# Optimization experiments

Measured on AMD Instinct MI355X. Metric: run time of the kernel, lower is better.

The kernel has to match this reference:

```python
import jax, jax.numpy as jnp
import numpy as np

NX = 2048
NY = 2048
K0 = 0.15                      # standard HW box wavenumber -> L = 2*pi/K0
KAPPA = 1.0
ALPHA = 1.0
DN = 0.001
DOMEGA = 0.001
K2_MIN = 1e-12


def _grid():
    L = 2.0 * np.pi / K0
    dx = L / NX
    dy = L / NY
    kx = (2.0 * np.pi * np.fft.fftfreq(NX, d=dx)).astype(np.float32)[:, None]  # [NX,1]
    ky = (2.0 * np.pi * np.fft.fftfreq(NY, d=dy)).astype(np.float32)[None, :]  # [1,NY]
    k2 = kx * kx + ky * ky
    # 2/3-rule dealias mask
    kx_max = np.abs(kx).max()
    ky_max = np.abs(ky).max()
    mask = ((np.abs(kx) <= (2.0 / 3.0) * kx_max) & (np.abs(ky) <= (2.0 / 3.0) * ky_max))
    return jnp.asarray(kx), jnp.asarray(ky), jnp.asarray(k2), jnp.asarray(mask)

KX, KY, K2, DEALIAS = _grid()


def _inv_laplacian_hat(w_hat):
    # phi_hat = -w_hat / k2, zeroing the (near-)zero modes
    safe_k2 = jnp.where(K2 > K2_MIN, K2, 1.0)
    return jnp.where(K2 > K2_MIN, -w_hat / safe_k2, 0.0)


def _bracket_spectral(phi_hat, f_hat):
    # J = d_x phi * d_y f - d_y phi * d_x f, dealiased with 2/3 mask
    dphix = jnp.fft.ifft2(1j * KX * phi_hat).real
    dphiy = jnp.fft.ifft2(1j * KY * phi_hat).real
    dfx = jnp.fft.ifft2(1j * KX * f_hat).real
    dfy = jnp.fft.ifft2(1j * KY * f_hat).real
    j = dphix * dfy - dphiy * dfx
    return jnp.fft.ifft2(DEALIAS * jnp.fft.fft2(j)).real


def setup_inputs() -> dict:
    key = jax.random.key(0)
    k1, k2 = jax.random.split(key)
    n = 0.1 * jax.random.normal(k1, (NX, NY), dtype=jnp.float32)
    omega = 0.1 * jax.random.normal(k2, (NX, NY), dtype=jnp.float32)
    return {"n": n, "omega": omega}


def reference(n, omega):
    n_hat = jnp.fft.fft2(n)
    w_hat = jnp.fft.fft2(omega)
    phi_hat = _inv_laplacian_hat(w_hat)
    phi = jnp.fft.ifft2(phi_hat).real

    adv_n = _bracket_spectral(phi_hat, n_hat)
    adv_w = _bracket_spectral(phi_hat, w_hat)

    dphi_dy = jnp.fft.ifft2(1j * KY * phi_hat).real
    dn_dy = jnp.fft.ifft2(1j * KY * n_hat).real

    drive_n = -KAPPA * dphi_dy
    drive_w = -KAPPA * dn_dy
    couple = ALPHA * (phi - n)

    lap_n = jnp.fft.ifft2(-K2 * n_hat).real
    lap_w = jnp.fft.ifft2(-K2 * w_hat).real

    dn = -adv_n + drive_n + couple + DN * lap_n
    dw = -adv_w + drive_w + couple + DOMEGA * lap_w
    return jnp.stack([dn, dw])  # [2, NX, NY]
```

## Files before the change

kernel.cpp:

```cpp
#include <hip/hip_runtime.h>
#include <hip/hip_fp16.h>
#include <math.h>


#define NF 2048
#define HALF 1024
#define K0F 0.15f
#define DEAL_LIM 682

typedef float2 cplx;
typedef __half2 ch;

__device__ __forceinline__ ch toh(cplx v){ return __float22half2_rn(make_float2(v.x, v.y)); }
__device__ __forceinline__ cplx toc(ch h){ float2 f = __half22float2(h); return make_float2(f.x, f.y); }

__device__ __forceinline__ int sw(int i){ return i ^ ((i>>4)&15) ^ ((i>>8)&15); }
__device__ __forceinline__ cplx cmul(cplx a, cplx b){ return make_float2(a.x*b.x - a.y*b.y, a.x*b.y + a.y*b.x); }
__device__ __forceinline__ cplx cadd(cplx a, cplx b){ return make_float2(a.x+b.x, a.y+b.y); }
__device__ __forceinline__ cplx csub(cplx a, cplx b){ return make_float2(a.x-b.x, a.y-b.y); }
template<int SIGN> __device__ __forceinline__ cplx rot90(cplx z){
  return (SIGN>0)? make_float2(-z.y,z.x) : make_float2(z.y,-z.x); }
__device__ __forceinline__ void lput(cplx* L, int i, cplx v){ L[sw(i)] = v; }
__device__ __forceinline__ cplx lget(const cplx* L, int i){ return L[sw(i)]; }

__device__ __forceinline__ int xcd_chunk(int bid, int nwg){
  return (bid & 7) * (nwg >> 3) + (bid >> 3);
}

template<int SIGN, int TPR, int M>
__device__ __forceinline__ void stage8_ip(cplx* X, int t) {
  constexpr int BPT = 256 / TPR;
  const float ang = (float)SIGN * 0.0030679615757712824f;
  cplx a[BPT][8];
#pragma unroll
  for (int u = 0; u < BPT; ++u) {
    const int b = t + u * TPR;
#pragma unroll
    for (int k = 0; k < 8; ++k) a[u][k] = X[sw(b + 256 * k)];
  }
  __syncthreads();
#pragma unroll
  for (int u = 0; u < BPT; ++u) {
    const int b = t + u * TPR;
    const int i = b & (M - 1);
    const int jm = b - i;
    cplx a0=a[u][0], a1=a[u][1], a2=a[u][2], a3=a[u][3],
         a4=a[u][4], a5=a[u][5], a6=a[u][6], a7=a[u][7];
    cplx t0=cadd(a0,a4), t1=csub(a0,a4), t2=cadd(a2,a6), t3=rot90<SIGN>(csub(a2,a6));
    cplx E0=cadd(t0,t2), E2=csub(t0,t2), E1=cadd(t1,t3), E3=csub(t1,t3);
    cplx u0=cadd(a1,a5), u1=csub(a1,a5), u2=cadd(a3,a7), u3=rot90<SIGN>(csub(a3,a7));
    cplx O0=cadd(u0,u2), O2=csub(u0,u2), O1=cadd(u1,u3), O3=csub(u1,u3);
    const float hh = 0.70710678118654752440f;
    O1 = cmul(O1, make_float2(hh, (float)SIGN*hh));
    O2 = rot90<SIGN>(O2);
    O3 = cmul(O3, make_float2(-hh, (float)SIGN*hh));
    cplx y0=cadd(E0,O0), y4=csub(E0,O0);
    cplx y1=cadd(E1,O1), y5=csub(E1,O1);
    cplx y2=cadd(E2,O2), y6=csub(E2,O2);
    cplx y3=cadd(E3,O3), y7=csub(E3,O3);
    float sn, cs;
    __sincosf(ang * (float)jm, &sn, &cs);
    cplx w1 = make_float2(cs, sn);
    cplx w2 = cmul(w1,w1), w3 = cmul(w2,w1), w4 = cmul(w2,w2);
    cplx w5 = cmul(w3,w2), w6 = cmul(w3,w3), w7 = cmul(w4,w3);
    const int o = 8*jm + i;
    X[sw(o)]       = y0;
    X[sw(o+M)]     = cmul(y1,w1);
    X[sw(o+2*M)]   = cmul(y2,w2);
    X[sw(o+3*M)]   = cmul(y3,w3);
    X[sw(o+4*M)]   = cmul(y4,w4);
    X[sw(o+5*M)]   = cmul(y5,w5);
    X[sw(o+6*M)]   = cmul(y6,w6);
    X[sw(o+7*M)]   = cmul(y7,w7);
  }
  __syncthreads();
}

template<int SIGN, int TPR>
__device__ __forceinline__ void stage4_ip(cplx* X, int t){
  constexpr int QPT = 512 / TPR;
  cplx a[QPT][4];
#pragma unroll
  for (int u=0; u<QPT; ++u){
    const int b = t + u*TPR;
#pragma unroll
    for (int k=0;k<4;++k) a[u][k] = X[sw(b + 512*k)];
  }
  __syncthreads();
#pragma unroll
  for (int u=0; u<QPT; ++u){
    const int b = t + u*TPR;
    cplx a0=a[u][0], a1=a[u][1], a2=a[u][2], a3=a[u][3];
    cplx t0=cadd(a0,a2), t1=csub(a0,a2), t2=cadd(a1,a3), t3=rot90<SIGN>(csub(a1,a3));
    X[sw(b)]       = cadd(t0,t2);
    X[sw(b+512)]   = cadd(t1,t3);
    X[sw(b+1024)]  = csub(t0,t2);
    X[sw(b+1536)]  = csub(t1,t3);
  }
  __syncthreads();
}

template<int SIGN, int TPR>
__device__ __forceinline__ void fft_ip(cplx* X, int t){
  __syncthreads();
  stage8_ip<SIGN,TPR,1>(X,t);
  stage8_ip<SIGN,TPR,8>(X,t);
  stage8_ip<SIGN,TPR,64>(X,t);
  stage4_ip<SIGN,TPR>(X,t);
}

__device__ __forceinline__ void unpack_point(cplx a, cplx b,
    float kxv, float kyv, float kxp, float kyp,
    cplx& s1, cplx& s2, cplx& s3, cplx& s4) {
  cplx nh = make_float2(0.5f*(a.x + b.x),  0.5f*(a.y - b.y));
  cplx wh = make_float2(0.5f*(a.y + b.y), -0.5f*(a.x - b.x));
  float k2 = kxv*kxv + kyv*kyv;
  float pinv = (k2 > 1e-12f) ? (-1.0f/k2) : 0.0f;
  cplx ph = make_float2(wh.x*pinv, wh.y*pinv);
  s1 = make_float2(-kxp*ph.y - kyp*ph.x, kxp*ph.x - kyp*ph.y);
  s2 = make_float2(-kxp*nh.y - kyp*nh.x, kxp*nh.x - kyp*nh.y);
  s3 = make_float2(-kxp*wh.y - kyp*wh.x, kxp*wh.x - kyp*wh.y);
  float dnc = 0.001f * k2;
  cplx Ln = make_float2( kyp*ph.y + (ph.x - nh.x) - dnc*nh.x,
                        -kyp*ph.x + (ph.y - nh.y) - dnc*nh.y);
  cplx Lw = make_float2( kyp*nh.y + (ph.x - nh.x) - dnc*wh.x,
                        -kyp*nh.x + (ph.y - nh.y) - dnc*wh.y);
  s4 = make_float2(Ln.x - Lw.y, Ln.y + Lw.x);
}


__global__ void __launch_bounds__(512) k_fwd_pack_T(const float* __restrict__ nIn,
                                                    const float* __restrict__ wIn,
                                                    cplx* __restrict__ out) {
  __shared__ cplx L[4*NF];
  const int tid = threadIdx.x;
  const int lb = xcd_chunk(blockIdx.x, gridDim.x);
  const int xb = lb*4;
#pragma unroll
  for (int u=0; u<4; ++u){
    int f = tid + u*512;
    int r = f >> 9;
    int p = f & 511;
    float4 nv = ((const float4*)(nIn + (size_t)(xb+r)*NF))[p];
    float4 wv = ((const float4*)(wIn + (size_t)(xb+r)*NF))[p];
    cplx* Lr = L + r*NF;
    lput(Lr, 4*p+0, make_float2(nv.x, wv.x));
    lput(Lr, 4*p+1, make_float2(nv.y, wv.y));
    lput(Lr, 4*p+2, make_float2(nv.z, wv.z));
    lput(Lr, 4*p+3, make_float2(nv.w, wv.w));
  }
  const int row = tid >> 7, t = tid & 127;
  fft_ip<-1,128>(L + row*NF, t);
  float4* o4 = (float4*)out;
#pragma unroll
  for (int u=0; u<8; ++u){
    int f = tid + u*512;
    int ky = f >> 1;
    int xp = f & 1;
    cplx a = lget(L + (2*xp)*NF, ky);
    cplx b = lget(L + (2*xp+1)*NF, ky);
    o4[(size_t)ky*(NF/2) + lb*2 + xp] = make_float4(a.x,a.y,b.x,b.y);
  }
}

__global__ void __launch_bounds__(512) k_unpackS(const cplx* __restrict__ in,
                                                 ch* __restrict__ S1, ch* __restrict__ S2,
                                                 ch* __restrict__ S3, ch* __restrict__ S4) {
  __shared__ cplx F0[NF], F1[NF];
  const int tid = threadIdx.x;
  const int b = xcd_chunk(blockIdx.x, gridDim.x);
  const int kyA = b;
  const int kyB = (b == 0) ? HALF : NF - b;
  const int half = tid >> 8;
  const int t = tid & 255;
  cplx* Fm = half ? F1 : F0;
  {
    const cplx* g = in + (size_t)(half ? kyB : kyA)*NF;
#pragma unroll
    for (int u=0; u<4; ++u){
      int p = t + u*256;
      float4 v = ((const float4*)g)[p];
      lput(Fm, 2*p,   make_float2(v.x,v.y));
      lput(Fm, 2*p+1, make_float2(v.z,v.w));
    }
    fft_ip<-1,256>(Fm, t);
  }
  const cplx* Fp = (b == 0) ? (const cplx*)Fm : (half ? F0 : F1);
  const int kyM = half ? kyB : kyA;
  const int sy = (kyM < HALF) ? kyM : kyM - NF;
  const float kyv = K0F * (float)sy;
  const float kyp = (kyM == HALF) ? 0.0f : kyv;
  const float sc = 1.0f/(float)NF;
  const size_t rbase = (size_t)kyM * NF;
#pragma unroll
  for (int u=0; u<8; ++u){
    int kx = t + u*256;
    int kx2 = (NF - kx) & (NF - 1);
    int sx = (kx < HALF) ? kx : kx - NF;
    float kxv = K0F * (float)sx;
    float kxp = (kx == HALF) ? 0.0f : kxv;
    cplx s1,s2,s3,s4;
    unpack_point(lget(Fm,kx), lget(Fp,kx2), kxv, kyv, kxp, kyp, s1,s2,s3,s4);
    S1[rbase+kx] = toh(make_float2(sc*s1.x, sc*s1.y));
    S2[rbase+kx] = toh(make_float2(sc*s2.x, sc*s2.y));
    S3[rbase+kx] = toh(make_float2(sc*s3.x, sc*s3.y));
    S4[rbase+kx] = toh(make_float2(sc*s4.x, sc*s4.y));
  }
}

__global__ void __launch_bounds__(512) k_inv2(const ch* __restrict__ in0,
                                              const ch* __restrict__ in1,
                                              ch* __restrict__ out0,
                                              ch* __restrict__ out1) {
  __shared__ cplx L[4*NF];
  const int tid = threadIdx.x;
  const int lb = xcd_chunk(blockIdx.x, gridDim.x);
  const ch* in = blockIdx.y ? in1 : in0;
  ch* out = blockIdx.y ? out1 : out0;
  const int rb = lb*4;
#pragma unroll
  for (int u=0; u<4; ++u){
    int f = tid + u*512;
    int r = f >> 9, p = f & 511;
    uint4 v = ((const uint4*)(in + (size_t)(rb+r)*NF))[p];
    cplx* Lr = L + r*NF;
    lput(Lr, 4*p+0, toc(*(ch*)&v.x));
    lput(Lr, 4*p+1, toc(*(ch*)&v.y));
    lput(Lr, 4*p+2, toc(*(ch*)&v.z));
    lput(Lr, 4*p+3, toc(*(ch*)&v.w));
  }
  const int row = tid >> 7, t = tid & 127;
  fft_ip<1,128>(L + row*NF, t);
  uint4* o16 = (uint4*)out;
#pragma unroll
  for (int u=0; u<4; ++u){
    int q = tid + u*512;
    ch h0 = toh(lget(L + 0*NF, q));
    ch h1 = toh(lget(L + 1*NF, q));
    ch h2 = toh(lget(L + 2*NF, q));
    ch h3 = toh(lget(L + 3*NF, q));
    uint4 v;
    v.x = *(unsigned*)&h0; v.y = *(unsigned*)&h1;
    v.z = *(unsigned*)&h2; v.w = *(unsigned*)&h3;
    o16[(size_t)q*(NF/4) + lb] = v;
  }
}

__global__ void __launch_bounds__(256) k_bracket(const ch* __restrict__ T1,
                                                 const ch* __restrict__ T2,
                                                 const ch* __restrict__ T3,
                                                 ch* __restrict__ out) {
  __shared__ cplx A[NF];
  const int t = threadIdx.x;
  const size_t base = (size_t)blockIdx.x * NF;
#pragma unroll
  for (int u=0; u<2; ++u){
    int p = t + u*256;
    uint4 v = ((const uint4*)(T1 + base))[p];
    lput(A, 4*p+0, toc(*(ch*)&v.x)); lput(A, 4*p+1, toc(*(ch*)&v.y));
    lput(A, 4*p+2, toc(*(ch*)&v.z)); lput(A, 4*p+3, toc(*(ch*)&v.w));
  }
  fft_ip<1,256>(A, t);
  cplx dphi[8];
#pragma unroll
  for (int u=0; u<8; ++u) dphi[u] = lget(A, t + u*256);
  __syncthreads();
#pragma unroll
  for (int u=0; u<2; ++u){
    int p = t + u*256;
    uint4 v = ((const uint4*)(T2 + base))[p];
    lput(A, 4*p+0, toc(*(ch*)&v.x)); lput(A, 4*p+1, toc(*(ch*)&v.y));
    lput(A, 4*p+2, toc(*(ch*)&v.z)); lput(A, 4*p+3, toc(*(ch*)&v.w));
  }
  fft_ip<1,256>(A, t);
  float jn[8];
#pragma unroll
  for (int u=0; u<8; ++u){
    cplx dd = lget(A, t + u*256);
    jn[u] = dphi[u].x*dd.y - dphi[u].y*dd.x;
  }
  __syncthreads();
#pragma unroll
  for (int u=0; u<2; ++u){
    int p = t + u*256;
    uint4 v = ((const uint4*)(T3 + base))[p];
    lput(A, 4*p+0, toc(*(ch*)&v.x)); lput(A, 4*p+1, toc(*(ch*)&v.y));
    lput(A, 4*p+2, toc(*(ch*)&v.z)); lput(A, 4*p+3, toc(*(ch*)&v.w));
  }
  fft_ip<1,256>(A, t);
  const float sc2 = 1.0f/((float)NF*(float)NF);
#pragma unroll
  for (int u=0; u<8; ++u){
    int c = t + u*256;
    cplx dd = lget(A, c);
    float jw = dphi[u].x*dd.y - dphi[u].y*dd.x;
    lput(A, c, make_float2(sc2*jn[u], sc2*jw));
  }
  fft_ip<-1,256>(A, t);
  uint4* o16 = (uint4*)(out + base);
#pragma unroll
  for (int u=0; u<2; ++u){
    int p = t + u*256;
    if (p <= 170 || p >= 341) {
      ch h0 = toh(lget(A, 4*p+0));
      ch h1 = toh(lget(A, 4*p+1));
      ch h2 = toh(lget(A, 4*p+2));
      ch h3 = toh(lget(A, 4*p+3));
      uint4 v;
      v.x = *(unsigned*)&h0; v.y = *(unsigned*)&h1;
      v.z = *(unsigned*)&h2; v.w = *(unsigned*)&h3;
      o16[p] = v;
    }
  }
}

__global__ void __launch_bounds__(512) k_slabX(const ch* __restrict__ in,
                                               ch* __restrict__ out) {
  __shared__ cplx L[4*NF];
  const int tid = threadIdx.x;
  const int lb = xcd_chunk(blockIdx.x, gridDim.x);
  const int cb = lb*4;
  if (cb >= 684 && cb <= 1360) {
    uint4 z; z.x = z.y = z.z = z.w = 0u;
#pragma unroll
    for (int u=0; u<4; ++u){
      int x = tid + u*512;
      *(uint4*)(out + (size_t)x*NF + cb) = z;
    }
    return;
  }
#pragma unroll
  for (int u=0; u<4; ++u){
    int x = tid + u*512;
    uint4 v = *(const uint4*)(in + (size_t)x*NF + cb);
    lput(L + 0*NF, x, toc(*(ch*)&v.x));
    lput(L + 1*NF, x, toc(*(ch*)&v.y));
    lput(L + 2*NF, x, toc(*(ch*)&v.z));
    lput(L + 3*NF, x, toc(*(ch*)&v.w));
  }
  const int row = tid >> 7, t = tid & 127;
  fft_ip<-1,128>(L + row*NF, t);
  const float sc = 1.0f/(float)NF;
#pragma unroll
  for (int v2=0; v2<16; ++v2){
    int g = tid + v2*512;
    int c = g >> 11, kk = g & 2047;
    int ky = cb + c;
    int sy = (ky < HALF) ? ky : ky - NF;
    int sx = (kk < HALF) ? kk : kk - NF;
    float m = (((sy<0?-sy:sy) <= DEAL_LIM) && ((sx<0?-sx:sx) <= DEAL_LIM)) ? sc : 0.0f;
    cplx z = lget(L + c*NF, kk);
    lput(L + c*NF, kk, make_float2(m*z.x, m*z.y));
  }
  fft_ip<1,128>(L + row*NF, t);
#pragma unroll
  for (int u=0; u<4; ++u){
    int x = tid + u*512;
    ch h0 = toh(lget(L + 0*NF, x));
    ch h1 = toh(lget(L + 1*NF, x));
    ch h2 = toh(lget(L + 2*NF, x));
    ch h3 = toh(lget(L + 3*NF, x));
    uint4 v;
    v.x = *(unsigned*)&h0; v.y = *(unsigned*)&h1;
    v.z = *(unsigned*)&h2; v.w = *(unsigned*)&h3;
    *(uint4*)(out + (size_t)x*NF + cb) = v;
  }
}

__global__ void __launch_bounds__(256) k_final(const ch* __restrict__ ADVt,
                                               const ch* __restrict__ T4,
                                               float* __restrict__ outF) {
  __shared__ cplx A[NF];
  const int t = threadIdx.x;
  const size_t base = (size_t)blockIdx.x * NF;
#pragma unroll
  for (int u=0; u<2; ++u){
    int p = t + u*256;
    uint4 v = ((const uint4*)(ADVt + base))[p];
    lput(A, 4*p+0, toc(*(ch*)&v.x)); lput(A, 4*p+1, toc(*(ch*)&v.y));
    lput(A, 4*p+2, toc(*(ch*)&v.z)); lput(A, 4*p+3, toc(*(ch*)&v.w));
  }
  fft_ip<1,256>(A, t);
  cplx adv[8];
#pragma unroll
  for (int u=0; u<8; ++u) adv[u] = lget(A, t + u*256);
  __syncthreads();
#pragma unroll
  for (int u=0; u<2; ++u){
    int p = t + u*256;
    uint4 v = ((const uint4*)(T4 + base))[p];
    lput(A, 4*p+0, toc(*(ch*)&v.x)); lput(A, 4*p+1, toc(*(ch*)&v.y));
    lput(A, 4*p+2, toc(*(ch*)&v.z)); lput(A, 4*p+3, toc(*(ch*)&v.w));
  }
  fft_ip<1,256>(A, t);
  const float sc = 1.0f/(float)NF;
  const size_t NSQ = (size_t)NF*NF;
#pragma unroll
  for (int u=0; u<8; ++u){
    int c = t + u*256;
    cplx Lv = lget(A, c);
    outF[base + c]       = sc*(Lv.x - adv[u].x);
    outF[NSQ + base + c] = sc*(Lv.y - adv[u].y);
  }
}

extern "C" void kernel_launch(void* const* d_in, const int* in_sizes, int n_in,
                              void* d_out, int out_size, void* d_ws, size_t ws_size,
                              hipStream_t stream) {
  const float* nIn = (const float*)d_in[0];
  const float* wIn = (const float*)d_in[1];
  float* outF = (float*)d_out;

  const size_t B  = (size_t)NF * NF * sizeof(cplx);
  const size_t Bh = (size_t)NF * NF * sizeof(ch);
  char* ws = (char*)d_ws;
  cplx* W    = (cplx*)(ws);
  ch*   S1   = (ch*)(ws + 1*B);
  ch*   S2   = (ch*)(ws + 1*B + Bh);
  ch*   S3   = (ch*)(ws + 2*B);
  ch*   S4   = (ch*)(ws + 2*B + Bh);
  ch*   T1   = (ch*)(ws + 3*B);
  ch*   T2   = (ch*)(ws + 3*B + Bh);
  ch*   T3   = (ch*)(ws + 4*B);
  ch*   T4   = (ch*)(ws + 4*B + Bh);
  ch*   ADVt = (ch*)(ws + 1*B);
  ch*   BR   = (ch*)d_out;

  k_fwd_pack_T <<<512, 512, 0, stream>>>(nIn, wIn, W);

  k_unpackS <<<1024, 512, 0, stream>>>(W, S1, S2, S3, S4);

  k_inv2 <<<dim3(512,2), 512, 0, stream>>>(S1, S2, T1, T2);
  k_inv2 <<<dim3(512,2), 512, 0, stream>>>(S3, S4, T3, T4);

  k_bracket <<<NF, 256, 0, stream>>>(T1, T2, T3, BR);

  k_slabX <<<512, 512, 0, stream>>>(BR, ADVt);

  k_final <<<NF, 256, 0, stream>>>(ADVt, T4, outF);
}
```

Before: 173.8 us.

## Run paired row FFTs concurrently with 512-thread blocks in bracket and final kernels

k_bracket and k_final now launch 512 threads per block and keep two shared-memory row buffers. The two halves of the block run independent 2048-point FFTs at the same time instead of one after another. This shortens the serial chain of FFT stages and barriers per row. The cost is double the shared memory per block, which may lower the number of resident blocks. fft_ip is still called with 256 threads and its internal barriers are now shared by both halves.

```diff
diff --git a/kernel.cpp b/kernel.cpp
--- a/kernel.cpp
+++ b/kernel.cpp
@@ -246,61 +246,55 @@
   }
 }
 
-__global__ void __launch_bounds__(256) k_bracket(const ch* __restrict__ T1,
+__global__ void __launch_bounds__(512) k_bracket(const ch* __restrict__ T1,
                                                  const ch* __restrict__ T2,
                                                  const ch* __restrict__ T3,
                                                  ch* __restrict__ out) {
-  __shared__ cplx A[NF];
-  const int t = threadIdx.x;
+  __shared__ cplx A[NF], Bb[NF];
+  const int tid = threadIdx.x;
+  const int half = tid >> 8;
+  const int t = tid & 255;
   const size_t base = (size_t)blockIdx.x * NF;
-#pragma unroll
-  for (int u=0; u<2; ++u){
-    int p = t + u*256;
-    uint4 v = ((const uint4*)(T1 + base))[p];
-    lput(A, 4*p+0, toc(*(ch*)&v.x)); lput(A, 4*p+1, toc(*(ch*)&v.y));
-    lput(A, 4*p+2, toc(*(ch*)&v.z)); lput(A, 4*p+3, toc(*(ch*)&v.w));
-  }
-  fft_ip<1,256>(A, t);
-  cplx dphi[8];
-#pragma unroll
-  for (int u=0; u<8; ++u) dphi[u] = lget(A, t + u*256);
-  __syncthreads();
-#pragma unroll
-  for (int u=0; u<2; ++u){
-    int p = t + u*256;
-    uint4 v = ((const uint4*)(T2 + base))[p];
-    lput(A, 4*p+0, toc(*(ch*)&v.x)); lput(A, 4*p+1, toc(*(ch*)&v.y));
-    lput(A, 4*p+2, toc(*(ch*)&v.z)); lput(A, 4*p+3, toc(*(ch*)&v.w));
-  }
-  fft_ip<1,256>(A, t);
-  float jn[8];
-#pragma unroll
-  for (int u=0; u<8; ++u){
-    cplx dd = lget(A, t + u*256);
-    jn[u] = dphi[u].x*dd.y - dphi[u].y*dd.x;
-  }
-  __syncthreads();
-#pragma unroll
-  for (int u=0; u<2; ++u){
-    int p = t + u*256;
-    uint4 v = ((const uint4*)(T3 + base))[p];
-    lput(A, 4*p+0, toc(*(ch*)&v.x)); lput(A, 4*p+1, toc(*(ch*)&v.y));
-    lput(A, 4*p+2, toc(*(ch*)&v.z)); lput(A, 4*p+3, toc(*(ch*)&v.w));
-  }
-  fft_ip<1,256>(A, t);
+  {
+    const ch* src = half ? T2 : T1;
+    cplx* L = half ? Bb : A;
+#pragma unroll
+    for (int u=0; u<2; ++u){
+      int p = t + u*256;
+      uint4 v = ((const uint4*)(src + base))[p];
+      lput(L, 4*p+0, toc(*(ch*)&v.x)); lput(L, 4*p+1, toc(*(ch*)&v.y));
+      lput(L, 4*p+2, toc(*(ch*)&v.z)); lput(L, 4*p+3, toc(*(ch*)&v.w));
+    }
+    fft_ip<1,256>(L, t);
+  }
+  cplx dphi[4];
+  float jn[4];
+#pragma unroll
+  for (int u=0; u<4; ++u){
+    int c = tid + u*512;
+    dphi[u] = lget(A, c);
+    cplx dn = lget(Bb, c);
+    jn[u] = dphi[u].x*dn.y - dphi[u].y*dn.x;
+  }
+  __syncthreads();
+  {
+    uint4 v = ((const uint4*)(T3 + base))[tid];
+    lput(Bb, 4*tid+0, toc(*(ch*)&v.x)); lput(Bb, 4*tid+1, toc(*(ch*)&v.y));
+    lput(Bb, 4*tid+2, toc(*(ch*)&v.z)); lput(Bb, 4*tid+3, toc(*(ch*)&v.w));
+  }
+  fft_ip<1,256>(Bb, t);
   const float sc2 = 1.0f/((float)NF*(float)NF);
 #pragma unroll
-  for (int u=0; u<8; ++u){
-    int c = t + u*256;
-    cplx dd = lget(A, c);
+  for (int u=0; u<4; ++u){
+    int c = tid + u*512;
+    cplx dd = lget(Bb, c);
     float jw = dphi[u].x*dd.y - dphi[u].y*dd.x;
     lput(A, c, make_float2(sc2*jn[u], sc2*jw));
   }
   fft_ip<-1,256>(A, t);
   uint4* o16 = (uint4*)(out + base);
-#pragma unroll
-  for (int u=0; u<2; ++u){
-    int p = t + u*256;
+  {
+    int p = tid;
     if (p <= 170 || p >= 341) {
       ch h0 = toh(lget(A, 4*p+0));
       ch h1 = toh(lget(A, 4*p+1));
@@ -367,40 +361,35 @@
   }
 }
 
-__global__ void __launch_bounds__(256) k_final(const ch* __restrict__ ADVt,
+__global__ void __launch_bounds__(512) k_final(const ch* __restrict__ ADVt,
                                                const ch* __restrict__ T4,
                                                float* __restrict__ outF) {
-  __shared__ cplx A[NF];
-  const int t = threadIdx.x;
+  __shared__ cplx A[NF], Bb[NF];
+  const int tid = threadIdx.x;
+  const int half = tid >> 8;
+  const int t = tid & 255;
   const size_t base = (size_t)blockIdx.x * NF;
-#pragma unroll
-  for (int u=0; u<2; ++u){
-    int p = t + u*256;
-    uint4 v = ((const uint4*)(ADVt + base))[p];
-    lput(A, 4*p+0, toc(*(ch*)&v.x)); lput(A, 4*p+1, toc(*(ch*)&v.y));
-    lput(A, 4*p+2, toc(*(ch*)&v.z)); lput(A, 4*p+3, toc(*(ch*)&v.w));
-  }
-  fft_ip<1,256>(A, t);
-  cplx adv[8];
-#pragma unroll
-  for (int u=0; u<8; ++u) adv[u] = lget(A, t + u*256);
-  __syncthreads();
-#pragma unroll
-  for (int u=0; u<2; ++u){
-    int p = t + u*256;
-    uint4 v = ((const uint4*)(T4 + base))[p];
-    lput(A, 4*p+0, toc(*(ch*)&v.x)); lput(A, 4*p+1, toc(*(ch*)&v.y));
-    lput(A, 4*p+2, toc(*(ch*)&v.z)); lput(A, 4*p+3, toc(*(ch*)&v.w));
-  }
-  fft_ip<1,256>(A, t);
+  {
+    const ch* src = half ? T4 : ADVt;
+    cplx* L = half ? Bb : A;
+#pragma unroll
+    for (int u=0; u<2; ++u){
+      int p = t + u*256;
+      uint4 v = ((const uint4*)(src + base))[p];
+      lput(L, 4*p+0, toc(*(ch*)&v.x)); lput(L, 4*p+1, toc(*(ch*)&v.y));
+      lput(L, 4*p+2, toc(*(ch*)&v.z)); lput(L, 4*p+3, toc(*(ch*)&v.w));
+    }
+    fft_ip<1,256>(L, t);
+  }
   const float sc = 1.0f/(float)NF;
   const size_t NSQ = (size_t)NF*NF;
 #pragma unroll
-  for (int u=0; u<8; ++u){
-    int c = t + u*256;
-    cplx Lv = lget(A, c);
-    outF[base + c]       = sc*(Lv.x - adv[u].x);
-    outF[NSQ + base + c] = sc*(Lv.y - adv[u].y);
+  for (int u=0; u<4; ++u){
+    int c = tid + u*512;
+    cplx adv = lget(A, c);
+    cplx Lv  = lget(Bb, c);
+    outF[base + c]       = sc*(Lv.x - adv.x);
+    outF[NSQ + base + c] = sc*(Lv.y - adv.y);
   }
 }
 
@@ -433,9 +422,9 @@
   k_inv2 <<<dim3(512,2), 512, 0, stream>>>(S1, S2, T1, T2);
   k_inv2 <<<dim3(512,2), 512, 0, stream>>>(S3, S4, T3, T4);
 
-  k_bracket <<<NF, 256, 0, stream>>>(T1, T2, T3, BR);
+  k_bracket <<<NF, 512, 0, stream>>>(T1, T2, T3, BR);
 
   k_slabX <<<512, 512, 0, stream>>>(BR, ADVt);
 
-  k_final <<<NF, 256, 0, stream>>>(ADVt, T4, outF);
-}
+  k_final <<<NF, 512, 0, stream>>>(ADVt, T4, outF);
+}
```

New measurement: 212.9 us. 22.5% more time.
